# Kernel optimization log

Measured on AMD Instinct MI355X. Metric: run time of the kernel, lower is better.

Reference implementation:

```python
import jax, jax.numpy as jnp
import numpy as np

B, Q, T, C = 2, 300, 25, 256
NH, NL, NP = 8, 4, 4
DFF = 1024
HD = C // NH
SHAPES = [(128, 128), (64, 64), (32, 32), (16, 16)]  # (H_l, W_l) per level
S = sum(h * w for h, w in SHAPES)
LQ = Q * T


def setup_inputs() -> dict:
    key = jax.random.key(0)
    ks = jax.random.split(key, 16)
    rn = lambda k, shape, s=0.02: jax.random.normal(k, shape, jnp.float32) * s
    starts = np.cumsum([0] + [h * w for h, w in SHAPES[:-1]])
    return {
        "tgt_text": jax.random.normal(ks[0], (B, Q, T, C), jnp.float32),
        "query_pos_text": jax.random.normal(ks[1], (B, Q, T, C), jnp.float32),
        "reference_points": jax.random.uniform(ks[2], (B, LQ, NL, 2), jnp.float32),
        "src": jax.random.normal(ks[3], (B, S, C), jnp.float32),
        "src_spatial_shapes": jnp.array(SHAPES, jnp.int32),
        "level_start_index": jnp.array(starts, jnp.int32),
        "in_proj_w": rn(ks[4], (3 * C, C)), "in_proj_b": jnp.zeros((3 * C,), jnp.float32),
        "out_proj_w": rn(ks[5], (C, C)), "out_proj_b": jnp.zeros((C,), jnp.float32),
        "ln1_g": jnp.ones((C,), jnp.float32), "ln1_b": jnp.zeros((C,), jnp.float32),
        "samp_off_w": rn(ks[6], (NH * NL * NP * 2, C)), "samp_off_b": rn(ks[7], (NH * NL * NP * 2,), 0.5),
        "aw_w": rn(ks[8], (NH * NL * NP, C)), "aw_b": jnp.zeros((NH * NL * NP,), jnp.float32),
        "vp_w": rn(ks[9], (C, C)), "vp_b": jnp.zeros((C,), jnp.float32),
        "op_w": rn(ks[10], (C, C)), "op_b": jnp.zeros((C,), jnp.float32),
        "ln2_g": jnp.ones((C,), jnp.float32), "ln2_b": jnp.zeros((C,), jnp.float32),
        "ffn1_w": rn(ks[11], (DFF, C)), "ffn1_b": jnp.zeros((DFF,), jnp.float32),
        "ffn2_w": rn(ks[12], (C, DFF)), "ffn2_b": jnp.zeros((C,), jnp.float32),
        "ln3_g": jnp.ones((C,), jnp.float32), "ln3_b": jnp.zeros((C,), jnp.float32),
    }


def _ln(x, g, b):
    m = jnp.mean(x, axis=-1, keepdims=True)
    v = jnp.var(x, axis=-1, keepdims=True)
    return (x - m) / jnp.sqrt(v + 1e-5) * g + b


def _self_attn(tgt, pos, in_proj_w, in_proj_b, out_proj_w, out_proj_b):
    # torch nn.MultiheadAttention math: q,k carry pos, v is raw tgt
    qk = (tgt + pos).reshape(B * Q, T, C)
    x = tgt.reshape(B * Q, T, C)
    Wq, Wk, Wv = jnp.split(in_proj_w, 3, axis=0)
    bq, bk, bv = jnp.split(in_proj_b, 3, axis=0)
    heads = lambda t: t.reshape(B * Q, T, NH, HD).transpose(0, 2, 1, 3)
    q = heads(qk @ Wq.T + bq)
    k = heads(qk @ Wk.T + bk)
    v = heads(x @ Wv.T + bv)
    attn = jax.nn.softmax(jnp.einsum("bhqd,bhkd->bhqk", q, k) / jnp.sqrt(jnp.float32(HD)), axis=-1)
    o = jnp.einsum("bhqk,bhkd->bhqd", attn, v).transpose(0, 2, 1, 3).reshape(B * Q, T, C)
    return (o @ out_proj_w.T + out_proj_b).reshape(B, Q, T, C)


def _ms_deform_attn(query, reference_points, src, shapes, samp_off_w, samp_off_b, aw_w, aw_b, vp_w, vp_b, op_w, op_b):
    # query: [B, LQ, C]; src: [B, S, C]
    value = (src @ vp_w.T + vp_b).reshape(B, S, NH, HD)
    off = (query @ samp_off_w.T + samp_off_b).reshape(B, LQ, NH, NL, NP, 2)
    aw = jax.nn.softmax((query @ aw_w.T + aw_b).reshape(B, LQ, NH, NL * NP), axis=-1)
    aw = aw.reshape(B, LQ, NH, NL, NP)
    # normalizer is (W_l, H_l)
    norm = jnp.array([[w, h] for (h, w) in shapes], jnp.float32)
    loc = reference_points[:, :, None, :, None, :] + off / norm[None, None, None, :, None, :]
    starts = np.cumsum([0] + [h * w for h, w in shapes])
    accum = jnp.zeros((B, NH, LQ, HD), jnp.float32)
    for l, (Hl, Wl) in enumerate(shapes):
        vl = value[:, starts[l]:starts[l] + Hl * Wl].transpose(0, 2, 1, 3)  # [B,NH,HW,HD]
        # grid_sample align_corners=False pixel coords
        xl = (loc[:, :, :, l, :, 0] * Wl - 0.5).transpose(0, 2, 1, 3).reshape(B, NH, LQ * NP)
        yl = (loc[:, :, :, l, :, 1] * Hl - 0.5).transpose(0, 2, 1, 3).reshape(B, NH, LQ * NP)
        x0 = jnp.floor(xl); y0 = jnp.floor(yl)
        wx1 = xl - x0; wy1 = yl - y0
        x0i = x0.astype(jnp.int32); y0i = y0.astype(jnp.int32)
        samp = jnp.zeros((B, NH, LQ * NP, HD), jnp.float32)
        for dx, dy, w in ((0, 0, (1 - wx1) * (1 - wy1)), (1, 0, wx1 * (1 - wy1)),
                          (0, 1, (1 - wx1) * wy1), (1, 1, wx1 * wy1)):
            xi = x0i + dx; yi = y0i + dy
            valid = (xi >= 0) & (xi < Wl) & (yi >= 0) & (yi < Hl)
            lin = jnp.clip(yi, 0, Hl - 1) * Wl + jnp.clip(xi, 0, Wl - 1)
            g = jnp.take_along_axis(vl, lin[..., None], axis=2)  # [B,NH,LQ*NP,HD]
            samp = samp + g * (w * valid)[..., None]
        samp = samp.reshape(B, NH, LQ, NP, HD)
        awl = aw[:, :, :, l, :].transpose(0, 2, 1, 3)  # [B,NH,LQ,NP]
        accum = accum + jnp.sum(samp * awl[..., None], axis=3)
    out = accum.transpose(0, 2, 1, 3).reshape(B, LQ, C)
    return out @ op_w.T + op_b


def reference(tgt_text, query_pos_text, reference_points, src, src_spatial_shapes, level_start_index,
              in_proj_w, in_proj_b, out_proj_w, out_proj_b, ln1_g, ln1_b,
              samp_off_w, samp_off_b, aw_w, aw_b, vp_w, vp_b, op_w, op_b, ln2_g, ln2_b,
              ffn1_w, ffn1_b, ffn2_w, ffn2_b, ln3_g, ln3_b):
    shapes = [tuple(int(v) for v in row) for row in np.asarray(src_spatial_shapes)]  # static
    # --- intra-text self-attention ---
    tgt2 = _self_attn(tgt_text, query_pos_text, in_proj_w, in_proj_b, out_proj_w, out_proj_b)
    tgt = _ln(tgt_text + tgt2, ln1_g, ln1_b)
    # --- multi-scale deformable cross-attention ---
    query = (tgt + query_pos_text).reshape(B, LQ, C)
    cross = _ms_deform_attn(query, reference_points, src, shapes,
                            samp_off_w, samp_off_b, aw_w, aw_b, vp_w, vp_b, op_w, op_b)
    tgt = _ln(tgt + cross.reshape(B, Q, T, C), ln2_g, ln2_b)
    # --- FFN ---
    ffn = jax.nn.relu(tgt @ ffn1_w.T + ffn1_b) @ ffn2_w.T + ffn2_b
    return _ln(tgt + ffn, ln3_g, ln3_b)
```

## Files before the change

kernel.cpp:

```cpp
#include <hip/hip_runtime.h>
#include <cstddef>

#define B_ 2
#define Q_ 300
#define T_ 25
#define C_ 256
#define NH_ 8
#define NL_ 4
#define NP_ 4
#define HD_ 32
#define DFF_ 1024
#define LQ_ (Q_ * T_)
#define NTOK_ (B_ * LQ_)
#define S_ 21760
#define BS_ (B_ * S_)

typedef __bf16 bf16x8 __attribute__((ext_vector_type(8)));
typedef float floatx4 __attribute__((ext_vector_type(4)));
typedef unsigned short ushort_t;

__device__ __forceinline__ unsigned pack_bf16(float x, float y) {
    unsigned ux = __float_as_uint(x) + 0x8000u;
    unsigned uy = __float_as_uint(y) + 0x8000u;
    return (ux >> 16) | (uy & 0xFFFF0000u);
}
__device__ __forceinline__ ushort_t f2bf_s(float x) {
    return (ushort_t)((__float_as_uint(x) + 0x8000u) >> 16);
}
__device__ __forceinline__ float bf2f(ushort_t u) {
    return __uint_as_float((unsigned)u << 16);
}

#define WOFF_IP   0
#define WOFF_OUT  196608
#define WOFF_VP   262144
#define WOFF_SO   327680
#define WOFF_AW   393216
#define WOFF_OP   425984
#define WOFF_F1   491520
#define WOFF_F2   753664
#define WTOTAL    1015808

__global__ __launch_bounds__(256) void convw_kernel(
    const float* __restrict__ ipw, const float* __restrict__ outw,
    const float* __restrict__ vpw, const float* __restrict__ sampw,
    const float* __restrict__ aww, const float* __restrict__ opw,
    const float* __restrict__ f1w, const float* __restrict__ f2w,
    ushort_t* __restrict__ dst)
{
    long long g = ((long long)blockIdx.x * 256 + threadIdx.x) * 8;
    if (g >= WTOTAL) return;
    const float* src; long long off;
    if      (g < WOFF_OUT) { src = ipw;   off = WOFF_IP; }
    else if (g < WOFF_VP)  { src = outw;  off = WOFF_OUT; }
    else if (g < WOFF_SO)  { src = vpw;   off = WOFF_VP; }
    else if (g < WOFF_AW)  { src = sampw; off = WOFF_SO; }
    else if (g < WOFF_OP)  { src = aww;   off = WOFF_AW; }
    else if (g < WOFF_F1)  { src = opw;   off = WOFF_OP; }
    else if (g < WOFF_F2)  { src = f1w;   off = WOFF_F1; }
    else                   { src = f2w;   off = WOFF_F2; }
    const float4* s4 = (const float4*)(src + (g - off));
    float4 a = s4[0], b = s4[1];
    uint4 o;
    o.x = pack_bf16(a.x, a.y); o.y = pack_bf16(a.z, a.w);
    o.z = pack_bf16(b.x, b.y); o.w = pack_bf16(b.z, b.w);
    *(uint4*)(dst + g) = o;
}

#define GBN 128
#define GBK 64
#define LDA_S 72

template<int AMODE, int OUTMODE, int GBMT>
__global__ __launch_bounds__(256) void gemm_w(
    const void* __restrict__ Av, const float* __restrict__ A2,
    const ushort_t* __restrict__ W,
    const float* __restrict__ bias, const float* __restrict__ bias2, int N1,
    void* __restrict__ Cv, long long partStride,
    int M, int N, int K, int kChunk, int ldc, int relu)
{
    constexpr int LA = GBMT / 16;
    constexpr int LB = 8;
    constexpr int WM = GBMT / 2;
    constexpr int NI = WM / 16;

    __shared__ unsigned short SH[GBMT * LDA_S + GBN * LDA_S];
    unsigned short* Asl = SH;
    unsigned short* Bsl = SH + GBMT * LDA_S;

    const int m0 = blockIdx.x * GBMT;
    if (m0 >= M) return;
    const int n0 = blockIdx.y * GBN;
    const int z  = blockIdx.z;
    const int kbeg = z * kChunk;
    const int kend = min(K, kbeg + kChunk);

    const int t  = threadIdx.x;
    const int wid  = t >> 6;
    const int lane = t & 63;
    const int wm = (wid >> 1) * WM;
    const int wn = (wid & 1) * 64;
    const int fm = lane & 15;
    const int fq = (lane >> 4) * 8;

    const bool addA2 = (AMODE == 1) && (n0 < N1);

    floatx4 acc[NI][4];
    #pragma unroll
    for (int i = 0; i < NI; ++i)
        #pragma unroll
        for (int j = 0; j < 4; ++j)
            acc[i][j] = (floatx4){0.f, 0.f, 0.f, 0.f};

    float4 pa[LA];
    uint2  pab[LA];
    uint2  pwb[LB];
    const float* Af = (const float*)Av;
    const ushort_t* Ab = (const ushort_t*)Av;

    auto load_tiles = [&](int k0) {
        #pragma unroll
        for (int i = 0; i < LA; ++i) {
            int idx = t + 256 * i;
            int row = idx >> 4;
            int c4  = (idx & 15) * 4;
            int gm = m0 + row;
            if constexpr (AMODE == 2) {
                uint2 v = {0u, 0u};
                if (gm < M) v = *(const uint2*)(Ab + (size_t)gm * K + k0 + c4);
                pab[i] = v;
            } else {
                float4 v = make_float4(0.f, 0.f, 0.f, 0.f);
                if (gm < M) {
                    v = *(const float4*)(Af + (size_t)gm * K + k0 + c4);
                    if constexpr (AMODE == 1) {
                        if (addA2) {
                            float4 v2 = *(const float4*)(A2 + (size_t)gm * K + k0 + c4);
                            v.x += v2.x; v.y += v2.y; v.z += v2.z; v.w += v2.w;
                        }
                    }
                }
                pa[i] = v;
            }
        }
        #pragma unroll
        for (int i = 0; i < LB; ++i) {
            int idx = t + 256 * i;
            int row = idx >> 4;
            int c4  = (idx & 15) * 4;
            pwb[i] = *(const uint2*)(W + (size_t)(n0 + row) * K + k0 + c4);
        }
    };

    load_tiles(kbeg);
    for (int k0 = kbeg; k0 < kend; k0 += GBK) {
        #pragma unroll
        for (int i = 0; i < LA; ++i) {
            int idx = t + 256 * i;
            int row = idx >> 4;
            int c4  = (idx & 15) * 4;
            if constexpr (AMODE == 2) {
                *(uint2*)&Asl[row * LDA_S + c4] = pab[i];
            } else {
                uint2 p;
                p.x = pack_bf16(pa[i].x, pa[i].y);
                p.y = pack_bf16(pa[i].z, pa[i].w);
                *(uint2*)&Asl[row * LDA_S + c4] = p;
            }
        }
        #pragma unroll
        for (int i = 0; i < LB; ++i) {
            int idx = t + 256 * i;
            int row = idx >> 4;
            int c4  = (idx & 15) * 4;
            *(uint2*)&Bsl[row * LDA_S + c4] = pwb[i];
        }
        __syncthreads();
        if (k0 + GBK < kend) load_tiles(k0 + GBK);

        #pragma unroll
        for (int kk = 0; kk < 2; ++kk) {
            bf16x8 af[NI], bfr[4];
            #pragma unroll
            for (int i = 0; i < NI; ++i)
                af[i] = *(const bf16x8*)&Asl[(wm + i * 16 + fm) * LDA_S + kk * 32 + fq];
            #pragma unroll
            for (int j = 0; j < 4; ++j)
                bfr[j] = *(const bf16x8*)&Bsl[(wn + j * 16 + fm) * LDA_S + kk * 32 + fq];

            #pragma unroll
            for (int i = 0; i < NI; ++i)
                #pragma unroll
                for (int j = 0; j < 4; ++j)
                    acc[i][j] = __builtin_amdgcn_mfma_f32_16x16x32_bf16(af[i], bfr[j], acc[i][j], 0, 0, 0);
        }
        __syncthreads();
    }

    float* Cf = (float*)Cv + (long long)z * partStride;
    ushort_t* Cb = (ushort_t*)Cv;
    const int cr = (lane >> 4) * 4;
    const int cc = lane & 15;

    if constexpr (OUTMODE == 0) {
        #pragma unroll
        for (int j = 0; j < 4; ++j) {
            int gn = n0 + wn + j * 16 + cc;
            float bia = 0.f;
            if (z == 0) bia = (bias2 && gn >= N1) ? bias2[gn - N1] : bias[gn];
            #pragma unroll
            for (int i = 0; i < NI; ++i)
                #pragma unroll
                for (int r = 0; r < 4; ++r) {
                    int gm = m0 + wm + i * 16 + cr + r;
                    if (gm < M) {
                        float v = acc[i][j][r] + bia;
                        if (relu) v = fmaxf(v, 0.f);
                        Cf[(size_t)gm * ldc + gn] = v;
                    }
                }
        }
    } else {
        unsigned short* epi = SH + wid * (WM * 64);
        #pragma unroll
        for (int j = 0; j < 4; ++j) {
            int gn = n0 + wn + j * 16 + cc;
            float bia = (bias2 && gn >= N1) ? bias2[gn - N1] : bias[gn];
            #pragma unroll
            for (int i = 0; i < NI; ++i)
                #pragma unroll
                for (int r = 0; r < 4; ++r) {
                    float v = acc[i][j][r] + bia;
                    if (relu) v = fmaxf(v, 0.f);
                    epi[(i * 16 + cr + r) * 64 + j * 16 + cc] = f2bf_s(v);
                }
        }
        #pragma unroll
        for (int pass = 0; pass < WM / 8; ++pass) {
            int lr = pass * 8 + (lane >> 3);
            int gm = m0 + wm + lr;
            uint4 vv = *(const uint4*)&epi[lr * 64 + (lane & 7) * 8];
            if (gm < M) {
                if constexpr (OUTMODE == 1) {
                    *(uint4*)&Cb[(size_t)gm * ldc + n0 + wn + (lane & 7) * 8] = vv;
                } else {
                    int bb = gm >= S_;
                    int s  = gm - bb * S_;
                    int gh = n0 + wn + (lane & 7) * 8;
                    *(uint4*)&Cb[(((size_t)(bb * 8 + (gh >> 5))) * S_ + s) * 32 + (gh & 31)] = vv;
                }
            }
        }
    }
}

template<int KSTEPS>
__global__ __launch_bounds__(256) void gemm_ln(
    const ushort_t* __restrict__ Ab,
    const ushort_t* __restrict__ W,
    const float* __restrict__ bias,
    const float* x,
    const float* __restrict__ g, const float* __restrict__ bv_,
    const float* __restrict__ pos,
    float* outp, float* qout, int M)
{
    constexpr int K = KSTEPS * 64;
    __shared__ unsigned short SH[(64 + 256) * LDA_S];
    unsigned short* Asl = SH;
    unsigned short* Bsl = SH + 64 * LDA_S;

    const int m0 = blockIdx.x * 64;
    if (m0 >= M) return;

    const int t    = threadIdx.x;
    const int wid  = t >> 6;
    const int lane = t & 63;
    const int wm   = wid * 16;
    const int fm   = lane & 15;
    const int fq   = (lane >> 4) * 8;

    floatx4 acc[16];
    #pragma unroll
    for (int j = 0; j < 16; ++j) acc[j] = (floatx4){0.f, 0.f, 0.f, 0.f};

    uint2 pab[4];
    uint2 pwb[16];

    auto load_tiles = [&](int k0) {
        #pragma unroll
        for (int i = 0; i < 4; ++i) {
            int idx = t + 256 * i;
            int row = idx >> 4;
            int c4  = (idx & 15) * 4;
            int gm  = m0 + row;
            uint2 v = {0u, 0u};
            if (gm < M) v = *(const uint2*)(Ab + (size_t)gm * K + k0 + c4);
            pab[i] = v;
        }
        #pragma unroll
        for (int i = 0; i < 16; ++i) {
            int idx = t + 256 * i;
            int row = idx >> 4;
            int c4  = (idx & 15) * 4;
            pwb[i] = *(const uint2*)(W + (size_t)row * K + k0 + c4);
        }
    };

    load_tiles(0);
    #pragma unroll 1
    for (int ks = 0; ks < KSTEPS; ++ks) {
        #pragma unroll
        for (int i = 0; i < 4; ++i) {
            int idx = t + 256 * i;
            *(uint2*)&Asl[(idx >> 4) * LDA_S + (idx & 15) * 4] = pab[i];
        }
        #pragma unroll
        for (int i = 0; i < 16; ++i) {
            int idx = t + 256 * i;
            *(uint2*)&Bsl[(idx >> 4) * LDA_S + (idx & 15) * 4] = pwb[i];
        }
        __syncthreads();
        if (ks + 1 < KSTEPS) load_tiles((ks + 1) * 64);

        #pragma unroll
        for (int kk = 0; kk < 2; ++kk) {
            bf16x8 af = *(const bf16x8*)&Asl[(wm + fm) * LDA_S + kk * 32 + fq];
            #pragma unroll
            for (int j = 0; j < 16; ++j) {
                bf16x8 bfr = *(const bf16x8*)&Bsl[(j * 16 + fm) * LDA_S + kk * 32 + fq];
                acc[j] = __builtin_amdgcn_mfma_f32_16x16x32_bf16(af, bfr, acc[j], 0, 0, 0);
            }
        }
        __syncthreads();
    }

    const int cr = (lane >> 4) * 4;
    const int cc = lane & 15;
    float* ep = (float*)SH;
    float4 gv = *(const float4*)(g   + lane * 4);
    float4 bb = *(const float4*)(bv_ + lane * 4);

    #pragma unroll
    for (int half = 0; half < 2; ++half) {
        if ((wid >> 1) == half) {
            int rbase = wm & 31;
            #pragma unroll
            for (int j = 0; j < 16; ++j) {
                float bia = bias[j * 16 + cc];
                #pragma unroll
                for (int r = 0; r < 4; ++r)
                    ep[(rbase + cr + r) * 264 + j * 16 + cc] = acc[j][r] + bia;
            }
        }
        __syncthreads();

        #pragma unroll
        for (int pass = 0; pass < 8; ++pass) {
            int rl   = pass * 4 + wid;
            int grow = m0 + half * 32 + rl;
            float4 v = *(const float4*)&ep[rl * 264 + lane * 4];
            if (grow < M) {
                float4 xv = *(const float4*)(x + (size_t)grow * 256 + lane * 4);
                v.x += xv.x; v.y += xv.y; v.z += xv.z; v.w += xv.w;
            }
            float s  = v.x + v.y + v.z + v.w;
            float ss = v.x * v.x + v.y * v.y + v.z * v.z + v.w * v.w;
            #pragma unroll
            for (int m = 32; m; m >>= 1) {
                s  += __shfl_xor(s, m);
                ss += __shfl_xor(ss, m);
            }
            float mean = s * (1.f / 256.f);
            float var  = ss * (1.f / 256.f) - mean * mean;
            float rstd = rsqrtf(var + 1e-5f);
            float4 y;
            y.x = (v.x - mean) * rstd * gv.x + bb.x;
            y.y = (v.y - mean) * rstd * gv.y + bb.y;
            y.z = (v.z - mean) * rstd * gv.z + bb.z;
            y.w = (v.w - mean) * rstd * gv.w + bb.w;
            if (grow < M) {
                *(float4*)(outp + (size_t)grow * 256 + lane * 4) = y;
                if (qout) {
                    float4 pv = *(const float4*)(pos + (size_t)grow * 256 + lane * 4);
                    float4 q;
                    q.x = y.x + pv.x; q.y = y.y + pv.y; q.z = y.z + pv.z; q.w = y.w + pv.w;
                    *(float4*)(qout + (size_t)grow * 256 + lane * 4) = q;
                }
            }
        }
        __syncthreads();
    }
}

__global__ __launch_bounds__(64) void attn_kernel(
    const ushort_t* __restrict__ qkv,
    ushort_t* __restrict__ o)
{
    int sh = blockIdx.x;
    int s = sh >> 3, h = sh & 7;
    __shared__ float qs[T_][HD_], ks[T_][HD_], vs[T_][HD_];
    int t = threadIdx.x;

    for (int idx = t; idx < T_ * HD_; idx += 64) {
        int i = idx >> 5, d = idx & 31;
        size_t base = ((size_t)(s * T_ + i)) * 768 + h * HD_ + d;
        qs[i][d] = bf2f(qkv[base]);
        ks[i][d] = bf2f(qkv[base + 256]);
        vs[i][d] = bf2f(qkv[base + 512]);
    }
    __syncthreads();

    if (t < T_) {
        float sc[T_];
        float mx = -1e30f;
        #pragma unroll
        for (int j = 0; j < T_; ++j) {
            float dot = 0.f;
            #pragma unroll
            for (int d = 0; d < HD_; ++d) dot += qs[t][d] * ks[j][d];
            sc[j] = dot * 0.17677669529663687f;
            mx = fmaxf(mx, sc[j]);
        }
        float sum = 0.f;
        #pragma unroll
        for (int j = 0; j < T_; ++j) { sc[j] = __expf(sc[j] - mx); sum += sc[j]; }
        float inv = 1.f / sum;
        float out[HD_];
        #pragma unroll
        for (int d = 0; d < HD_; ++d) out[d] = 0.f;
        for (int j = 0; j < T_; ++j) {
            float p = sc[j] * inv;
            #pragma unroll
            for (int d = 0; d < HD_; ++d) out[d] += p * vs[j][d];
        }
        size_t ob = ((size_t)(s * T_ + t)) * C_ + h * HD_;
        #pragma unroll
        for (int d = 0; d < HD_; ++d) o[ob + d] = f2bf_s(out[d]);
    }
}

#define DCHUNK_ 118
__global__ __launch_bounds__(256, 4) void deform_kernel(
    const ushort_t* __restrict__ value,
    const float* __restrict__ d12,
    const float* __restrict__ refpts,
    ushort_t* __restrict__ out)
{
    const int bi    = blockIdx.x;
    const int xcd   = bi & 7;
    const int yy    = bi >> 3;
    const int combo = xcd + 8 * (yy & 1);
    const int chunk = yy >> 1;
    const int h     = combo & 7;
    const int b     = combo >> 3;

    __shared__ float tls[64][60];

    const int tid = threadIdx.x;
    const int t0  = chunk * 64;

    #pragma unroll
    for (int i = 0; i < 2; ++i) {
        int idx  = tid + 256 * i;
        int trw  = idx >> 3;
        int c4   = (idx & 7) * 4;
        int tl   = min(t0 + trw, LQ_ - 1);
        float4 v;
        v.x = __builtin_nontemporal_load(d12 + (size_t)(b * LQ_ + tl) * 384 + h * 32 + c4 + 0);
        v.y = __builtin_nontemporal_load(d12 + (size_t)(b * LQ_ + tl) * 384 + h * 32 + c4 + 1);
        v.z = __builtin_nontemporal_load(d12 + (size_t)(b * LQ_ + tl) * 384 + h * 32 + c4 + 2);
        v.w = __builtin_nontemporal_load(d12 + (size_t)(b * LQ_ + tl) * 384 + h * 32 + c4 + 3);
        *(float4*)&tls[trw][c4] = v;
    }
    {
        int trw = tid >> 2;
        int c4  = (tid & 3) * 4;
        int tl  = min(t0 + trw, LQ_ - 1);
        float4 v;
        v.x = __builtin_nontemporal_load(d12 + (size_t)(b * LQ_ + tl) * 384 + 256 + h * 16 + c4 + 0);
        v.y = __builtin_nontemporal_load(d12 + (size_t)(b * LQ_ + tl) * 384 + 256 + h * 16 + c4 + 1);
        v.z = __builtin_nontemporal_load(d12 + (size_t)(b * LQ_ + tl) * 384 + 256 + h * 16 + c4 + 2);
        v.w = __builtin_nontemporal_load(d12 + (size_t)(b * LQ_ + tl) * 384 + 256 + h * 16 + c4 + 3);
        *(float4*)&tls[trw][32 + c4] = v;
    }
    if (tid < 128) {
        int trw = tid >> 1;
        int c4  = (tid & 1) * 4;
        int tl  = min(t0 + trw, LQ_ - 1);
        float4 v;
        v.x = __builtin_nontemporal_load(refpts + (size_t)(b * LQ_ + tl) * 8 + c4 + 0);
        v.y = __builtin_nontemporal_load(refpts + (size_t)(b * LQ_ + tl) * 8 + c4 + 1);
        v.z = __builtin_nontemporal_load(refpts + (size_t)(b * LQ_ + tl) * 8 + c4 + 2);
        v.w = __builtin_nontemporal_load(refpts + (size_t)(b * LQ_ + tl) * 8 + c4 + 3);
        *(float4*)&tls[trw][48 + c4] = v;
    }
    __syncthreads();

    if (tid < 64) {
        float lg[16];
        float mx = -1e30f;
        #pragma unroll
        for (int i = 0; i < 16; ++i) { lg[i] = tls[tid][32 + i]; mx = fmaxf(mx, lg[i]); }
        float sum = 0.f;
        #pragma unroll
        for (int i = 0; i < 16; ++i) { lg[i] = __expf(lg[i] - mx); sum += lg[i]; }
        float inv = 1.f / sum;
        #pragma unroll
        for (int i = 0; i < 16; ++i) tls[tid][32 + i] = lg[i] * inv;
    }
    __syncthreads();

    const int wave = tid >> 6;
    const int lane = tid & 63;
    const int ti   = lane >> 2;
    const int d8   = (lane & 3) * 8;
    const int row  = wave * 16 + ti;

    int tl = t0 + row;
    const bool active = (tl < LQ_);
    tl = min(tl, LQ_ - 1);
    const int tok = b * LQ_ + tl;

    const int HW[4]     = {128, 64, 32, 16};
    const int starts[4] = {0, 16384, 20480, 21504};

    const ushort_t* vplane = value + (size_t)combo * ((size_t)S_ * HD_) + d8;
    const float* trow = tls[row];

    float accv[8];
    #pragma unroll
    for (int i = 0; i < 8; ++i) accv[i] = 0.f;

    #pragma unroll
    for (int l = 0; l < 4; ++l) {
        const int Hl = HW[l], Wl = HW[l];
        float rx = trow[48 + l * 2 + 0];
        float ry = trow[48 + l * 2 + 1];
        const ushort_t* vbase = vplane + (size_t)starts[l] * HD_;

        int   voff[16];
        float wgt[16];
        #pragma unroll
        for (int p = 0; p < 4; ++p) {
            float ox = trow[l * 8 + p * 2 + 0];
            float oy = trow[l * 8 + p * 2 + 1];
            float aww = trow[32 + l * 4 + p];
            float xl = rx * (float)Wl + ox - 0.5f;
            float yl = ry * (float)Hl + oy - 0.5f;
            float x0f = floorf(xl), y0f = floorf(yl);
            int x0 = (int)x0f, y0 = (int)y0f;
            float wx1 = xl - x0f, wy1 = yl - y0f;
            float wx0 = 1.f - wx1, wy0 = 1.f - wy1;
            #pragma unroll
            for (int c = 0; c < 4; ++c) {
                int dx = c & 1, dy = c >> 1;
                int xi = x0 + dx, yi = y0 + dy;
                float w = (dx ? wx1 : wx0) * (dy ? wy1 : wy0);
                bool valid = (xi >= 0) & (xi < Wl) & (yi >= 0) & (yi < Hl);
                int xc = min(max(xi, 0), Wl - 1);
                int yc = min(max(yi, 0), Hl - 1);
                voff[p * 4 + c] = yc * Wl + xc;
                wgt[p * 4 + c]  = (valid ? w : 0.f) * aww;
            }
        }
        uint4 raw[16];
        #pragma unroll
        for (int i = 0; i < 16; ++i)
            raw[i] = *(const uint4*)(vbase + (size_t)voff[i] * HD_);
        #pragma unroll
        for (int i = 0; i < 16; ++i) {
            float wc = wgt[i];
            accv[0] += __uint_as_float((raw[i].x & 0xFFFFu) << 16) * wc;
            accv[1] += __uint_as_float(raw[i].x & 0xFFFF0000u) * wc;
            accv[2] += __uint_as_float((raw[i].y & 0xFFFFu) << 16) * wc;
            accv[3] += __uint_as_float(raw[i].y & 0xFFFF0000u) * wc;
            accv[4] += __uint_as_float((raw[i].z & 0xFFFFu) << 16) * wc;
            accv[5] += __uint_as_float(raw[i].z & 0xFFFF0000u) * wc;
            accv[6] += __uint_as_float((raw[i].w & 0xFFFFu) << 16) * wc;
            accv[7] += __uint_as_float(raw[i].w & 0xFFFF0000u) * wc;
        }
    }
    if (active) {
        uint4 po;
        po.x = pack_bf16(accv[0], accv[1]);
        po.y = pack_bf16(accv[2], accv[3]);
        po.z = pack_bf16(accv[4], accv[5]);
        po.w = pack_bf16(accv[6], accv[7]);
        *(uint4*)(out + (size_t)tok * C_ + h * HD_ + d8) = po;
    }
}

extern "C" void kernel_launch(void* const* d_in, const int* in_sizes, int n_in,
                              void* d_out, int out_size, void* d_ws, size_t ws_size,
                              hipStream_t stream) {
    const float* tgt_text = (const float*)d_in[0];
    const float* pos      = (const float*)d_in[1];
    const float* refpts   = (const float*)d_in[2];
    const float* src      = (const float*)d_in[3];
    const float* in_proj_w  = (const float*)d_in[6];
    const float* in_proj_b  = (const float*)d_in[7];
    const float* out_proj_w = (const float*)d_in[8];
    const float* out_proj_b = (const float*)d_in[9];
    const float* ln1_g = (const float*)d_in[10];
    const float* ln1_b = (const float*)d_in[11];
    const float* samp_off_w = (const float*)d_in[12];
    const float* samp_off_b = (const float*)d_in[13];
    const float* aw_w = (const float*)d_in[14];
    const float* aw_b = (const float*)d_in[15];
    const float* vp_w = (const float*)d_in[16];
    const float* vp_b = (const float*)d_in[17];
    const float* op_w = (const float*)d_in[18];
    const float* op_b = (const float*)d_in[19];
    const float* ln2_g = (const float*)d_in[20];
    const float* ln2_b = (const float*)d_in[21];
    const float* ffn1_w = (const float*)d_in[22];
    const float* ffn1_b = (const float*)d_in[23];
    const float* ffn2_w = (const float*)d_in[24];
    const float* ffn2_b = (const float*)d_in[25];
    const float* ln3_g = (const float*)d_in[26];
    const float* ln3_b = (const float*)d_in[27];

    const long long NC = (long long)NTOK_ * C_;
    float* ws = (float*)d_ws;
    float* A    = ws;
    float* Bq   = ws + NC;
    float* Creg = ws + 2 * NC;
    float* D12  = Creg + (long long)NTOK_ * DFF_;
    float* E    = D12 + (long long)NTOK_ * 384;
    float* F    = E + NC;
    ushort_t* wb = (ushort_t*)(F + NC);

    ushort_t* qkv  = (ushort_t*)Creg;
    ushort_t* valt = (ushort_t*)Creg + (size_t)NTOK_ * 768;

    const int MB64P  = 240;
    const int MB128P = 120;
    const int MBV64  = BS_ / 64;

    convw_kernel<<<496, 256, 0, stream>>>(in_proj_w, out_proj_w, vp_w, samp_off_w,
                                          aw_w, op_w, ffn1_w, ffn2_w, wb);
    gemm_w<1, 1, 64><<<dim3(MB64P, 6, 1), 256, 0, stream>>>(tgt_text, pos, wb + WOFF_IP,
        in_proj_b, nullptr, 512, qkv, 0, NTOK_, 768, 256, 256, 768, 0);
    gemm_w<0, 2, 64><<<dim3(MBV64, 2, 1), 256, 0, stream>>>(src, nullptr, wb + WOFF_VP,
        vp_b, nullptr, 0, valt, 0, BS_, 256, 256, 256, 0, 0);
    attn_kernel<<<B_ * Q_ * NH_, 64, 0, stream>>>(qkv, (ushort_t*)E);
    gemm_ln<4><<<MB64P, 256, 0, stream>>>((ushort_t*)E, wb + WOFF_OUT, out_proj_b,
        tgt_text, ln1_g, ln1_b, pos, A, Bq, NTOK_);
    gemm_w<0, 0, 64><<<dim3(MB64P, 3, 1), 256, 0, stream>>>(Bq, nullptr, wb + WOFF_SO,
        samp_off_b, aw_b, 256, D12, 0, NTOK_, 384, 256, 256, 384, 0);
    deform_kernel<<<8 * 2 * DCHUNK_, 256, 0, stream>>>(valt, D12, refpts, (ushort_t*)E);
    gemm_ln<4><<<MB64P, 256, 0, stream>>>((ushort_t*)E, wb + WOFF_OP, op_b,
        A, ln2_g, ln2_b, nullptr, A, nullptr, NTOK_);
    gemm_w<0, 1, 128><<<dim3(MB128P, 8, 1), 256, 0, stream>>>(A, nullptr, wb + WOFF_F1,
        ffn1_b, nullptr, 0, Creg, 0, NTOK_, DFF_, 256, 256, DFF_, 1);
    gemm_ln<16><<<MB64P, 256, 0, stream>>>((ushort_t*)Creg, wb + WOFF_F2, ffn2_b,
        A, ln3_g, ln3_b, nullptr, (float*)d_out, nullptr, NTOK_);
}
```

Measured before the change: 377.2 us.

## Merge QKV and value-projection GEMMs into one launch; tune deform occupancy

Moves the GEMM body into a device function so that one kernel launch can dispatch blocks for either the QKV in-projection or the value projection, chosen by block index. This removes a kernel launch and lets the two independent GEMMs share the GPU at the same time, filling the tail of each. The deform kernel's launch-bounds occupancy hint drops from 4 to 3 waves-per-SIMD target, allowing more registers. A scheduling barrier is added so all 16 gathered loads are issued before any accumulation. The cost is a merged kernel whose register and LDS footprint must suit both GEMM variants, and fewer resident deform waves to hide load latency.

```diff
diff --git a/kernel.cpp b/kernel.cpp
--- a/kernel.cpp
+++ b/kernel.cpp
@@ -72,26 +72,27 @@
 #define LDA_S 72
 
 template<int AMODE, int OUTMODE, int GBMT>
-__global__ __launch_bounds__(256) void gemm_w(
+__device__ __forceinline__ void gemm_body(
+    int bx, int by, int bz,
     const void* __restrict__ Av, const float* __restrict__ A2,
     const ushort_t* __restrict__ W,
     const float* __restrict__ bias, const float* __restrict__ bias2, int N1,
     void* __restrict__ Cv, long long partStride,
-    int M, int N, int K, int kChunk, int ldc, int relu)
+    int M, int N, int K, int kChunk, int ldc, int relu,
+    unsigned short* SH)
 {
     constexpr int LA = GBMT / 16;
     constexpr int LB = 8;
     constexpr int WM = GBMT / 2;
     constexpr int NI = WM / 16;
 
-    __shared__ unsigned short SH[GBMT * LDA_S + GBN * LDA_S];
     unsigned short* Asl = SH;
     unsigned short* Bsl = SH + GBMT * LDA_S;
 
-    const int m0 = blockIdx.x * GBMT;
+    const int m0 = bx * GBMT;
     if (m0 >= M) return;
-    const int n0 = blockIdx.y * GBN;
-    const int z  = blockIdx.z;
+    const int n0 = by * GBN;
+    const int z  = bz;
     const int kbeg = z * kChunk;
     const int kend = min(K, kbeg + kChunk);
 
@@ -254,6 +255,38 @@
     }
 }
 
+template<int AMODE, int OUTMODE, int GBMT>
+__global__ __launch_bounds__(256) void gemm_w(
+    const void* __restrict__ Av, const float* __restrict__ A2,
+    const ushort_t* __restrict__ W,
+    const float* __restrict__ bias, const float* __restrict__ bias2, int N1,
+    void* __restrict__ Cv, long long partStride,
+    int M, int N, int K, int kChunk, int ldc, int relu)
+{
+    __shared__ unsigned short SH[GBMT * LDA_S + GBN * LDA_S];
+    gemm_body<AMODE, OUTMODE, GBMT>(blockIdx.x, blockIdx.y, blockIdx.z,
+        Av, A2, W, bias, bias2, N1, Cv, partStride, M, N, K, kChunk, ldc, relu, SH);
+}
+
+__global__ __launch_bounds__(256) void qkvvp_kernel(
+    const float* __restrict__ tgt, const float* __restrict__ pos,
+    const float* __restrict__ src,
+    const ushort_t* __restrict__ wip, const float* __restrict__ ipb,
+    const ushort_t* __restrict__ wvp, const float* __restrict__ vpb,
+    ushort_t* __restrict__ qkv, ushort_t* __restrict__ valt)
+{
+    __shared__ unsigned short SH[(64 + GBN) * LDA_S];
+    int bx = blockIdx.x;
+    if (bx < 240 * 6) {
+        gemm_body<1, 1, 64>(bx % 240, bx / 240, 0, tgt, pos, wip,
+                            ipb, nullptr, 512, qkv, 0, NTOK_, 768, 256, 256, 768, 0, SH);
+    } else {
+        int q = bx - 240 * 6;
+        gemm_body<0, 2, 64>(q % 680, q / 680, 0, src, nullptr, wvp,
+                            vpb, nullptr, 0, valt, 0, BS_, 256, 256, 256, 0, 0, SH);
+    }
+}
+
 template<int KSTEPS>
 __global__ __launch_bounds__(256) void gemm_ln(
     const ushort_t* __restrict__ Ab,
@@ -440,7 +473,7 @@
 }
 
 #define DCHUNK_ 118
-__global__ __launch_bounds__(256, 4) void deform_kernel(
+__global__ __launch_bounds__(256, 3) void deform_kernel(
     const ushort_t* __restrict__ value,
     const float* __restrict__ d12,
     const float* __restrict__ refpts,
@@ -567,6 +600,7 @@
         #pragma unroll
         for (int i = 0; i < 16; ++i)
             raw[i] = *(const uint4*)(vbase + (size_t)voff[i] * HD_);
+        __builtin_amdgcn_sched_barrier(0);
         #pragma unroll
         for (int i = 0; i < 16; ++i) {
             float wc = wgt[i];
@@ -635,14 +669,11 @@
 
     const int MB64P  = 240;
     const int MB128P = 120;
-    const int MBV64  = BS_ / 64;
 
     convw_kernel<<<496, 256, 0, stream>>>(in_proj_w, out_proj_w, vp_w, samp_off_w,
                                           aw_w, op_w, ffn1_w, ffn2_w, wb);
-    gemm_w<1, 1, 64><<<dim3(MB64P, 6, 1), 256, 0, stream>>>(tgt_text, pos, wb + WOFF_IP,
-        in_proj_b, nullptr, 512, qkv, 0, NTOK_, 768, 256, 256, 768, 0);
-    gemm_w<0, 2, 64><<<dim3(MBV64, 2, 1), 256, 0, stream>>>(src, nullptr, wb + WOFF_VP,
-        vp_b, nullptr, 0, valt, 0, BS_, 256, 256, 256, 0, 0);
+    qkvvp_kernel<<<240 * 6 + 680 * 2, 256, 0, stream>>>(tgt_text, pos, src,
+        wb + WOFF_IP, in_proj_b, wb + WOFF_VP, vp_b, qkv, valt);
     attn_kernel<<<B_ * Q_ * NH_, 64, 0, stream>>>(qkv, (ushort_t*)E);
     gemm_ln<4><<<MB64P, 256, 0, stream>>>((ushort_t*)E, wb + WOFF_OUT, out_proj_b,
         tgt_text, ln1_g, ln1_b, pos, A, Bq, NTOK_);
```

New measurement: 1.138 ms. 3.02x slower.
